# Kernel tuning notes

Hardware: AMD Instinct MI355X
Metric: run time of the kernel (lower is better)

The kernel has to match this reference:

```python
import jax, jax.numpy as jnp
import numpy as np

EMBED_DIM = 512
NUM_HEADS = 8
TGT_LEN = 2048
SRC_LEN = 2048
BSZ = 4
W_SCALE = 0.02  # keep pre-softmax logits in a sane range


def setup_inputs() -> dict:
    key = jax.random.key(0)
    ks = jax.random.split(key, 13)
    E = EMBED_DIM
    inp = {
        "query": jax.random.normal(ks[0], (TGT_LEN, BSZ, E), jnp.float32),
        "key": jax.random.normal(ks[1], (SRC_LEN, BSZ, E), jnp.float32),
        "value": jax.random.normal(ks[2], (SRC_LEN, BSZ, E), jnp.float32),
        "attn_mask": jax.random.normal(ks[3], (TGT_LEN, SRC_LEN), jnp.float32),
        # Linear params, torch layout: W is [out, in], y = x @ W.T + b
        "Wq": jax.random.normal(ks[4], (E, E), jnp.float32) * W_SCALE,
        "bq": jax.random.normal(ks[5], (E,), jnp.float32) * W_SCALE,
        "Wk": jax.random.normal(ks[6], (E, E), jnp.float32) * W_SCALE,
        "bk": jax.random.normal(ks[7], (E,), jnp.float32) * W_SCALE,
        "Wv": jax.random.normal(ks[8], (E, E), jnp.float32) * W_SCALE,
        "bv": jax.random.normal(ks[9], (E,), jnp.float32) * W_SCALE,
        "Wo": jax.random.normal(ks[10], (E, E), jnp.float32) * W_SCALE,
        "bo": jax.random.normal(ks[11], (E,), jnp.float32) * W_SCALE,
    }
    return inp


def reference(query, key, value, attn_mask, Wq, bq, Wk, bk, Wv, bv, Wo, bo):
    # QAT quant/dequant stubs are identity in float math; dropout p=0 (eval) is identity.
    T, B, E = query.shape
    S = key.shape[0]
    H = NUM_HEADS
    hd = E // H
    scale = hd ** (-0.5)

    q = query @ Wq.T + bq            # [T, B, E]
    k = key @ Wk.T + bk              # [S, B, E]
    v = value @ Wv.T + bv            # [S, B, E]

    q = q.reshape(T, B, H, hd) * scale
    k = k.reshape(S, B, H, hd)
    v = v.reshape(S, B, H, hd)

    # scores: [B, H, T, S]
    scores = jnp.einsum("tbhd,sbhd->bhts", q, k)
    scores = scores + attn_mask[None, None, :, :]  # mask_add.add (float mask)
    attn = jax.nn.softmax(scores, axis=-1)         # SegmentLUTSoftmax == softmax in float

    out = jnp.einsum("bhts,sbhd->tbhd", attn, v).reshape(T, B, E)
    out = out @ Wo.T + bo                          # out_proj

    # need_weights=True, average_attn_weights=True: mean over heads -> [B, T, S]
    attn_weights = jnp.sum(attn, axis=1) * (1.0 / H)
    return out, attn_weights
```

## Files before the change

### kernel.cpp

```cpp
#include <hip/hip_runtime.h>
#include <hip/hip_bf16.h>

#define T_LEN 2048
#define S_LEN 2048
#define BSZ   4
#define EMB   512
#define NHEAD 8
#define HDIM  64
#define L2E   1.44269504088896f

using bf16x8 = __attribute__((ext_vector_type(8))) short;
using f32x4  = __attribute__((ext_vector_type(4))) float;

static __device__ __forceinline__ unsigned short f2bf(float x) {
    __hip_bfloat16 h = __float2bfloat16(x);
    return *reinterpret_cast<unsigned short*>(&h);
}
static __device__ __forceinline__ float bf2f(unsigned short u) {
    __hip_bfloat16 h;
    *reinterpret_cast<unsigned short*>(&h) = u;
    return __bfloat162float(h);
}
static __device__ __forceinline__ unsigned int pk2(float a, float b) {
    return (unsigned)f2bf(a) | ((unsigned)f2bf(b) << 16);
}

__global__ __launch_bounds__(256) void convert_w4(
    const float* __restrict__ W0, const float* __restrict__ W1,
    const float* __restrict__ W2, const float* __restrict__ W3,
    unsigned short* __restrict__ Hi, unsigned short* __restrict__ Lo, int n4)
{
    const int z = blockIdx.y;
    const float* X = (z == 0) ? W0 : (z == 1) ? W1 : (z == 2) ? W2 : W3;
    unsigned short* H = Hi + (size_t)z * (size_t)EMB * EMB;
    unsigned short* L = Lo + (size_t)z * (size_t)EMB * EMB;
    const int stride = gridDim.x * 256;
    for (int i = blockIdx.x * 256 + threadIdx.x; i < n4; i += stride) {
        float4 v = ((const float4*)X)[i];
        unsigned short h0 = f2bf(v.x), h1 = f2bf(v.y), h2 = f2bf(v.z), h3 = f2bf(v.w);
        uint2 ph, pg;
        ph.x = (unsigned)h0 | ((unsigned)h1 << 16);
        ph.y = (unsigned)h2 | ((unsigned)h3 << 16);
        pg.x = pk2(v.x - bf2f(h0), v.y - bf2f(h1));
        pg.y = pk2(v.z - bf2f(h2), v.w - bf2f(h3));
        ((uint2*)H)[i] = ph;
        ((uint2*)L)[i] = pg;
    }
}

template <int MODE, bool XF32, bool SPLIT>
__global__ __launch_bounds__(256) void proj_mfma(
    const float* __restrict__ Xf,
    const unsigned short* __restrict__ Xhi, const unsigned short* __restrict__ Xlo,
    const unsigned short* __restrict__ Whi, const unsigned short* __restrict__ Wlo,
    const float* __restrict__ bias,
    float* __restrict__ Yf, unsigned short* __restrict__ Yhi, float scale)
{
    const int n0 = blockIdx.x * 64;
    const int m0 = blockIdx.y * 64;

    __shared__ unsigned short whs[64 * 64];
    __shared__ unsigned short wls[SPLIT ? 64 * 64 : 1];
    __shared__ unsigned short xhs[XF32 ? 64 * 64 : 1];
    __shared__ unsigned short xls[(XF32 && SPLIT) ? 64 * 64 : 1];

    const int tid = threadIdx.x;
    const int w   = tid >> 6;
    const int l   = tid & 63;
    const int l4  = l >> 4, l15 = l & 15;
    const int sw  = (l & 7) << 4;
    char* whsb = (char*)whs;
    char* wlsb = (char*)wls;
    char* xhsb = (char*)xhs;
    char* xlsb = (char*)xls;

    const int srow = tid >> 2;
    const int schk = tid & 3;
    const size_t wbase = (size_t)(n0 + srow) * 512 + schk * 16;
    const int stw = (srow * 128 + schk * 32) ^ ((srow & 7) << 4);

    f32x4 acc[4];
    #pragma unroll
    for (int nb = 0; nb < 4; ++nb) { f32x4 z = {0.f, 0.f, 0.f, 0.f}; acc[nb] = z; }

    uint4 wh0 = *(const uint4*)(Whi + wbase);
    uint4 wh1 = *(const uint4*)(Whi + wbase + 8);
    uint4 wl0, wl1;
    if constexpr (SPLIT) {
        wl0 = *(const uint4*)(Wlo + wbase);
        wl1 = *(const uint4*)(Wlo + wbase + 8);
    }

    const size_t xfbase = (size_t)(m0 + srow) * 512 + schk * 16;
    const size_t xbase  = (size_t)(m0 + w * 16 + l15) * 512 + l4 * 8;
    float4 xp0, xp1, xp2, xp3;
    bf16x8 ah0, ah1, al0, al1;
    if constexpr (XF32) {
        xp0 = *(const float4*)(Xf + xfbase);
        xp1 = *(const float4*)(Xf + xfbase + 4);
        xp2 = *(const float4*)(Xf + xfbase + 8);
        xp3 = *(const float4*)(Xf + xfbase + 12);
    } else {
        ah0 = *(const bf16x8*)(Xhi + xbase);
        ah1 = *(const bf16x8*)(Xhi + xbase + 32);
        if constexpr (SPLIT) {
            al0 = *(const bf16x8*)(Xlo + xbase);
            al1 = *(const bf16x8*)(Xlo + xbase + 32);
        }
    }

    for (int c = 0; c < 8; ++c) {
        __syncthreads();
        *(uint4*)(whsb + stw)        = wh0;
        *(uint4*)(whsb + (stw ^ 16)) = wh1;
        if constexpr (SPLIT) {
            *(uint4*)(wlsb + stw)        = wl0;
            *(uint4*)(wlsb + (stw ^ 16)) = wl1;
        }
        if constexpr (XF32) {
            uint4 H0, H1;
            H0.x = pk2(xp0.x, xp0.y); H0.y = pk2(xp0.z, xp0.w);
            H0.z = pk2(xp1.x, xp1.y); H0.w = pk2(xp1.z, xp1.w);
            H1.x = pk2(xp2.x, xp2.y); H1.y = pk2(xp2.z, xp2.w);
            H1.z = pk2(xp3.x, xp3.y); H1.w = pk2(xp3.z, xp3.w);
            *(uint4*)(xhsb + stw)        = H0;
            *(uint4*)(xhsb + (stw ^ 16)) = H1;
            if constexpr (SPLIT) {
                uint4 L0, L1;
                L0.x = pk2(xp0.x - bf2f(f2bf(xp0.x)), xp0.y - bf2f(f2bf(xp0.y)));
                L0.y = pk2(xp0.z - bf2f(f2bf(xp0.z)), xp0.w - bf2f(f2bf(xp0.w)));
                L0.z = pk2(xp1.x - bf2f(f2bf(xp1.x)), xp1.y - bf2f(f2bf(xp1.y)));
                L0.w = pk2(xp1.z - bf2f(f2bf(xp1.z)), xp1.w - bf2f(f2bf(xp1.w)));
                L1.x = pk2(xp2.x - bf2f(f2bf(xp2.x)), xp2.y - bf2f(f2bf(xp2.y)));
                L1.y = pk2(xp2.z - bf2f(f2bf(xp2.z)), xp2.w - bf2f(f2bf(xp2.w)));
                L1.z = pk2(xp3.x - bf2f(f2bf(xp3.x)), xp3.y - bf2f(f2bf(xp3.y)));
                L1.w = pk2(xp3.z - bf2f(f2bf(xp3.z)), xp3.w - bf2f(f2bf(xp3.w)));
                *(uint4*)(xlsb + stw)        = L0;
                *(uint4*)(xlsb + (stw ^ 16)) = L1;
            }
        }
        __syncthreads();

        bf16x8 cah[2], cal[2];
        if constexpr (XF32) {
            #pragma unroll
            for (int kc = 0; kc < 2; ++kc) {
                const int aoff = (((w * 16 + l15) * 128) + kc * 64 + l4 * 16) ^ sw;
                cah[kc] = *(const bf16x8*)(xhsb + aoff);
                if constexpr (SPLIT) cal[kc] = *(const bf16x8*)(xlsb + aoff);
            }
        } else {
            cah[0] = ah0; cah[1] = ah1;
            if constexpr (SPLIT) { cal[0] = al0; cal[1] = al1; }
        }

        if (c < 7) {
            const size_t wb2 = wbase + (size_t)(c + 1) * 64;
            wh0 = *(const uint4*)(Whi + wb2);
            wh1 = *(const uint4*)(Whi + wb2 + 8);
            if constexpr (SPLIT) {
                wl0 = *(const uint4*)(Wlo + wb2);
                wl1 = *(const uint4*)(Wlo + wb2 + 8);
            }
            if constexpr (XF32) {
                const size_t xb2 = xfbase + (size_t)(c + 1) * 64;
                xp0 = *(const float4*)(Xf + xb2);
                xp1 = *(const float4*)(Xf + xb2 + 4);
                xp2 = *(const float4*)(Xf + xb2 + 8);
                xp3 = *(const float4*)(Xf + xb2 + 12);
            } else {
                const size_t xb2 = xbase + (size_t)(c + 1) * 64;
                ah0 = *(const bf16x8*)(Xhi + xb2);
                ah1 = *(const bf16x8*)(Xhi + xb2 + 32);
                if constexpr (SPLIT) {
                    al0 = *(const bf16x8*)(Xlo + xb2);
                    al1 = *(const bf16x8*)(Xlo + xb2 + 32);
                }
            }
        }

        #pragma unroll
        for (int kc = 0; kc < 2; ++kc) {
            #pragma unroll
            for (int nb = 0; nb < 4; ++nb) {
                const int off = (((nb * 16 + l15) * 128) + kc * 64 + l4 * 16) ^ sw;
                bf16x8 bh = *(const bf16x8*)(whsb + off);
                acc[nb] = __builtin_amdgcn_mfma_f32_16x16x32_bf16(cah[kc], bh, acc[nb], 0, 0, 0);
                if constexpr (SPLIT) {
                    bf16x8 bl = *(const bf16x8*)(wlsb + off);
                    acc[nb] = __builtin_amdgcn_mfma_f32_16x16x32_bf16(cah[kc], bl, acc[nb], 0, 0, 0);
                    acc[nb] = __builtin_amdgcn_mfma_f32_16x16x32_bf16(cal[kc], bh, acc[nb], 0, 0, 0);
                }
            }
        }
    }

    #pragma unroll
    for (int nb = 0; nb < 4; ++nb)
        #pragma unroll
        for (int r = 0; r < 4; ++r) {
            const int m = m0 + w * 16 + l4 * 4 + r;
            const int n = n0 + nb * 16 + l15;
            const float y = (acc[nb][r] + bias[n]) * scale;
            const size_t idx = (size_t)m * 512 + n;
            if constexpr (MODE == 0) Yf[idx] = y;
            else                     Yhi[idx] = f2bf(y);
        }
}

__global__ __launch_bounds__(256) void transpose_v(const unsigned short* __restrict__ V,
                                                   unsigned short* __restrict__ Vt)
{
    const int s0 = blockIdx.x * 64;
    const int h  = blockIdx.y, b = blockIdx.z;
    __shared__ unsigned short tile[64][72];
    const int tid = threadIdx.x;
    {
        const int r = tid >> 2, c = (tid & 3) * 16;
        const unsigned short* src = V + ((size_t)(s0 + r) * BSZ + b) * EMB + h * HDIM + c;
        uint4 u0 = *(const uint4*)(src);
        uint4 u1 = *(const uint4*)(src + 8);
        *(uint4*)&tile[r][c]     = u0;
        *(uint4*)&tile[r][c + 8] = u1;
    }
    __syncthreads();
    {
        const int d = tid >> 2, sg = tid & 3;
        unsigned int w_[8];
        #pragma unroll
        for (int j = 0; j < 8; ++j) {
            unsigned int lo = tile[sg * 16 + 2 * j][d];
            unsigned int hi = tile[sg * 16 + 2 * j + 1][d];
            w_[j] = lo | (hi << 16);
        }
        uint4 o0 = {w_[0], w_[1], w_[2], w_[3]};
        uint4 o1 = {w_[4], w_[5], w_[6], w_[7]};
        unsigned short* dst = Vt + ((size_t)(b * NHEAD + h) * HDIM + d) * S_LEN + s0 + sg * 16;
        *(uint4*)dst       = o0;
        *(uint4*)(dst + 8) = o1;
    }
}

__global__ __launch_bounds__(256) void flash_fwd_mfma(
    const unsigned short* __restrict__ Qbf, const unsigned short* __restrict__ Kbf,
    const unsigned short* __restrict__ Vt,  const float* __restrict__ mask,
    unsigned short* __restrict__ Ohi, unsigned short* __restrict__ Olo,
    float* __restrict__ Lout)
{
    const int tt0 = blockIdx.x * 128;
    const int h   = blockIdx.y, b = blockIdx.z;

    __shared__ unsigned short ks[64 * 64];
    __shared__ unsigned short vs[64 * 64];
    __shared__ unsigned short pl[4][2][16 * 64];

    const int tid = threadIdx.x;
    const int w   = tid >> 6;
    const int l   = tid & 63;
    const int l4  = l >> 4, l15 = l & 15;
    const int sw  = (l & 7) << 4;

    char* ksb = (char*)ks;
    char* vsb = (char*)vs;
    char* pb_[2] = {(char*)pl[w][0], (char*)pl[w][1]};

    bf16x8 qf[2][2];
    #pragma unroll
    for (int a = 0; a < 2; ++a) {
        const int t = tt0 + w * 32 + a * 16 + l15;
        const unsigned short* qp = Qbf + ((size_t)t * BSZ + b) * EMB + h * HDIM + l4 * 8;
        qf[a][0] = *(const bf16x8*)(qp);
        qf[a][1] = *(const bf16x8*)(qp + 32);
    }

    f32x4 oacc[2][4];
    #pragma unroll
    for (int a = 0; a < 2; ++a)
        #pragma unroll
        for (int nb = 0; nb < 4; ++nb) { f32x4 z = {0.f, 0.f, 0.f, 0.f}; oacc[a][nb] = z; }
    float lsum[2] = {0.f, 0.f};

    const int srow = tid >> 2;
    const int schk = tid & 3;
    const unsigned short* kcol = Kbf + (size_t)b * EMB + h * HDIM + schk * 16;
    const unsigned short* vrow = Vt + ((size_t)(b * NHEAD + h) * HDIM + srow) * S_LEN + schk * 16;
    const int stw = (srow * 128 + schk * 32) ^ ((srow & 7) << 4);

    const float* mrowp[2];
    #pragma unroll
    for (int a = 0; a < 2; ++a)
        mrowp[a] = mask + (size_t)(tt0 + w * 32 + a * 16 + l15) * S_LEN + l4 * 4;

    const unsigned short* kp0 = kcol + (size_t)srow * BSZ * EMB;
    uint4 ka0 = *(const uint4*)(kp0);
    uint4 ka1 = *(const uint4*)(kp0 + 8);
    uint4 va0 = *(const uint4*)(vrow);
    uint4 va1 = *(const uint4*)(vrow + 8);

    for (int s0 = 0; s0 < S_LEN; s0 += 64) {
        __syncthreads();
        *(uint4*)(ksb + stw)        = ka0;
        *(uint4*)(ksb + (stw ^ 16)) = ka1;
        *(uint4*)(vsb + stw)        = va0;
        *(uint4*)(vsb + (stw ^ 16)) = va1;
        __syncthreads();

        if (s0 + 64 < S_LEN) {
            const unsigned short* kp2 = kcol + (size_t)(s0 + 64 + srow) * BSZ * EMB;
            ka0 = *(const uint4*)(kp2);
            ka1 = *(const uint4*)(kp2 + 8);
            va0 = *(const uint4*)(vrow + s0 + 64);
            va1 = *(const uint4*)(vrow + s0 + 64 + 8);
        }

        f32x4 sacc[2][4];
        #pragma unroll
        for (int a = 0; a < 2; ++a)
            #pragma unroll
            for (int nb = 0; nb < 4; ++nb) { f32x4 z = {0.f, 0.f, 0.f, 0.f}; sacc[a][nb] = z; }
        #pragma unroll
        for (int kc = 0; kc < 2; ++kc) {
            #pragma unroll
            for (int nb = 0; nb < 4; ++nb) {
                const int off = (((nb * 16 + l15) * 128) + kc * 64 + l4 * 16) ^ sw;
                bf16x8 kf = *(const bf16x8*)(ksb + off);
                sacc[0][nb] = __builtin_amdgcn_mfma_f32_16x16x32_bf16(kf, qf[0][kc], sacc[0][nb], 0, 0, 0);
                sacc[1][nb] = __builtin_amdgcn_mfma_f32_16x16x32_bf16(kf, qf[1][kc], sacc[1][nb], 0, 0, 0);
            }
        }

        #pragma unroll
        for (int a = 0; a < 2; ++a) {
            char* pw = pb_[a];
            #pragma unroll
            for (int nb = 0; nb < 4; ++nb) {
                float4 mk = *(const float4*)(mrowp[a] + s0 + nb * 16);
                const float p0 = __builtin_amdgcn_exp2f(fmaf(mk.x, L2E, sacc[a][nb][0]));
                const float p1 = __builtin_amdgcn_exp2f(fmaf(mk.y, L2E, sacc[a][nb][1]));
                const float p2 = __builtin_amdgcn_exp2f(fmaf(mk.z, L2E, sacc[a][nb][2]));
                const float p3 = __builtin_amdgcn_exp2f(fmaf(mk.w, L2E, sacc[a][nb][3]));
                lsum[a] += (p0 + p1) + (p2 + p3);
                uint2 pk;
                pk.x = pk2(p0, p1);
                pk.y = pk2(p2, p3);
                *(uint2*)(pw + ((l15 * 128 + nb * 32 + l4 * 8) ^ sw)) = pk;
            }
        }

        bf16x8 pa[2][2];
        #pragma unroll
        for (int a = 0; a < 2; ++a) {
            pa[a][0] = *(const bf16x8*)(pb_[a] + ((l15 * 128 + l4 * 16) ^ sw));
            pa[a][1] = *(const bf16x8*)(pb_[a] + ((l15 * 128 + 64 + l4 * 16) ^ sw));
        }
        #pragma unroll
        for (int nb = 0; nb < 4; ++nb) {
            const int off0 = (((nb * 16 + l15) * 128) + l4 * 16) ^ sw;
            bf16x8 vf0 = *(const bf16x8*)(vsb + off0);
            bf16x8 vf1 = *(const bf16x8*)(vsb + (off0 ^ 64));
            oacc[0][nb] = __builtin_amdgcn_mfma_f32_16x16x32_bf16(pa[0][0], vf0, oacc[0][nb], 0, 0, 0);
            oacc[0][nb] = __builtin_amdgcn_mfma_f32_16x16x32_bf16(pa[0][1], vf1, oacc[0][nb], 0, 0, 0);
            oacc[1][nb] = __builtin_amdgcn_mfma_f32_16x16x32_bf16(pa[1][0], vf0, oacc[1][nb], 0, 0, 0);
            oacc[1][nb] = __builtin_amdgcn_mfma_f32_16x16x32_bf16(pa[1][1], vf1, oacc[1][nb], 0, 0, 0);
        }
    }

    #pragma unroll
    for (int a = 0; a < 2; ++a) {
        float lfull = lsum[a];
        lfull += __shfl_xor(lfull, 16);
        lfull += __shfl_xor(lfull, 32);
        float linv[4];
        #pragma unroll
        for (int r = 0; r < 4; ++r)
            linv[r] = 1.0f / __shfl(lfull, l4 * 4 + r);

        #pragma unroll
        for (int nb = 0; nb < 4; ++nb)
            #pragma unroll
            for (int r = 0; r < 4; ++r) {
                const int t = tt0 + w * 32 + a * 16 + l4 * 4 + r;
                const size_t idx = ((size_t)t * BSZ + b) * EMB + h * HDIM + nb * 16 + l15;
                const float y = oacc[a][nb][r] * linv[r];
                const unsigned short hi = f2bf(y);
                Ohi[idx] = hi;
                Olo[idx] = f2bf(y - bf2f(hi));
            }
        if (l < 16)
            Lout[((size_t)b * NHEAD + h) * T_LEN + tt0 + w * 32 + a * 16 + l] = lfull;
    }
}

__global__ __launch_bounds__(256) void attn_weights_mfma(
    const unsigned short* __restrict__ Qhi, const unsigned short* __restrict__ Khi,
    const float* __restrict__ mask, const float* __restrict__ Lin,
    float* __restrict__ Wout)
{
    const int tt0 = blockIdx.x * 128;
    const int ss0 = blockIdx.y * 64;
    const int b   = blockIdx.z;

    __shared__ unsigned short khs[2][64 * 64];
    __shared__ float lls[NHEAD][128];

    const int tid = threadIdx.x;
    const int w   = tid >> 6;
    const int l   = tid & 63;
    const int l4  = l >> 4, l15 = l & 15;
    const int sw  = (l & 7) << 4;

    for (int i = tid; i < NHEAD * 128; i += 256) {
        const int hh = i >> 7, t2 = i & 127;
        lls[hh][t2] = (1.0f / NHEAD) / Lin[(size_t)(b * NHEAD + hh) * T_LEN + tt0 + t2];
    }

    float4 msk[2][4];
    #pragma unroll
    for (int a = 0; a < 2; ++a) {
        const float* mrowp = mask + (size_t)(tt0 + w * 32 + a * 16 + l15) * S_LEN + ss0 + l4 * 4;
        #pragma unroll
        for (int nb = 0; nb < 4; ++nb) msk[a][nb] = *(const float4*)(mrowp + nb * 16);
    }
    #pragma unroll
    for (int a = 0; a < 2; ++a)
        #pragma unroll
        for (int nb = 0; nb < 4; ++nb) {
            msk[a][nb].x *= L2E; msk[a][nb].y *= L2E;
            msk[a][nb].z *= L2E; msk[a][nb].w *= L2E;
        }

    float4 wacc[2][4] = {};

    const int srow = tid >> 2;
    const int schk = tid & 3;
    const size_t kbase = ((size_t)(ss0 + srow) * BSZ + b) * EMB + schk * 16;
    const int stw = (srow * 128 + schk * 32) ^ ((srow & 7) << 4);
    size_t qbase[2];
    #pragma unroll
    for (int a = 0; a < 2; ++a)
        qbase[a] = ((size_t)(tt0 + w * 32 + a * 16 + l15) * BSZ + b) * EMB + l4 * 8;

    {
        uint4 a0 = *(const uint4*)(Khi + kbase);
        uint4 a1 = *(const uint4*)(Khi + kbase + 8);
        char* k0 = (char*)khs[0];
        *(uint4*)(k0 + stw)        = a0;
        *(uint4*)(k0 + (stw ^ 16)) = a1;
    }
    __syncthreads();

    uint4 kh0, kh1;

    for (int h = 0; h < NHEAD; ++h) {
        const int cur = h & 1;
        char* khsb = (char*)khs[cur];
        const bool haveNext = (h + 1 < NHEAD);

        if (haveNext) {
            kh0 = *(const uint4*)(Khi + kbase + (h + 1) * HDIM);
            kh1 = *(const uint4*)(Khi + kbase + (h + 1) * HDIM + 8);
        }

        bf16x8 qh[2][2];
        #pragma unroll
        for (int a = 0; a < 2; ++a) {
            qh[a][0] = *(const bf16x8*)(Qhi + qbase[a] + h * HDIM);
            qh[a][1] = *(const bf16x8*)(Qhi + qbase[a] + h * HDIM + 32);
        }

        f32x4 sacc[2][4];
        #pragma unroll
        for (int a = 0; a < 2; ++a)
            #pragma unroll
            for (int nb = 0; nb < 4; ++nb) { f32x4 z = {0.f, 0.f, 0.f, 0.f}; sacc[a][nb] = z; }
        #pragma unroll
        for (int kc = 0; kc < 2; ++kc) {
            #pragma unroll
            for (int nb = 0; nb < 4; ++nb) {
                const int off = (((nb * 16 + l15) * 128) + kc * 64 + l4 * 16) ^ sw;
                bf16x8 kf = *(const bf16x8*)(khsb + off);
                sacc[0][nb] = __builtin_amdgcn_mfma_f32_16x16x32_bf16(kf, qh[0][kc], sacc[0][nb], 0, 0, 0);
                sacc[1][nb] = __builtin_amdgcn_mfma_f32_16x16x32_bf16(kf, qh[1][kc], sacc[1][nb], 0, 0, 0);
            }
        }

        #pragma unroll
        for (int a = 0; a < 2; ++a) {
            const float lh = lls[h][w * 32 + a * 16 + l15];
            #pragma unroll
            for (int nb = 0; nb < 4; ++nb) {
                wacc[a][nb].x += __builtin_amdgcn_exp2f(sacc[a][nb][0] + msk[a][nb].x) * lh;
                wacc[a][nb].y += __builtin_amdgcn_exp2f(sacc[a][nb][1] + msk[a][nb].y) * lh;
                wacc[a][nb].z += __builtin_amdgcn_exp2f(sacc[a][nb][2] + msk[a][nb].z) * lh;
                wacc[a][nb].w += __builtin_amdgcn_exp2f(sacc[a][nb][3] + msk[a][nb].w) * lh;
            }
        }

        if (haveNext) {
            char* kn = (char*)khs[cur ^ 1];
            *(uint4*)(kn + stw)        = kh0;
            *(uint4*)(kn + (stw ^ 16)) = kh1;
        }
        __syncthreads();
    }

    #pragma unroll
    for (int a = 0; a < 2; ++a) {
        float* orow = Wout + ((size_t)b * T_LEN + tt0 + w * 32 + a * 16 + l15) * S_LEN + ss0 + l4 * 4;
        #pragma unroll
        for (int nb = 0; nb < 4; ++nb)
            *(float4*)(orow + nb * 16) = wacc[a][nb];
    }
}

extern "C" void kernel_launch(void* const* d_in, const int* in_sizes, int n_in,
                              void* d_out, int out_size, void* d_ws, size_t ws_size,
                              hipStream_t stream)
{
    const float* query = (const float*)d_in[0];
    const float* key   = (const float*)d_in[1];
    const float* value = (const float*)d_in[2];
    const float* mask  = (const float*)d_in[3];
    const float* Wq    = (const float*)d_in[4];
    const float* bq    = (const float*)d_in[5];
    const float* Wk    = (const float*)d_in[6];
    const float* bk    = (const float*)d_in[7];
    const float* Wv    = (const float*)d_in[8];
    const float* bv    = (const float*)d_in[9];
    const float* Wo    = (const float*)d_in[10];
    const float* bo    = (const float*)d_in[11];

    float* out = (float*)d_out;

    const size_t NQKV = (size_t)T_LEN * BSZ * EMB;
    const size_t NW   = (size_t)EMB * EMB;

    unsigned short* qhi = (unsigned short*)d_ws;
    unsigned short* khi = qhi + NQKV;
    unsigned short* vhi = khi + NQKV;
    unsigned short* whb = vhi + NQKV;
    unsigned short* wlb = whb + 4 * NW;
    float* lb = (float*)(wlb + 4 * NW);

    unsigned short* wqh = whb + 0 * NW;
    unsigned short* wkh = whb + 1 * NW;
    unsigned short* wvh = whb + 2 * NW;
    unsigned short* woh = whb + 3 * NW, *wol = wlb + 3 * NW;

    unsigned short* vt  = (unsigned short*)(out + NQKV);
    unsigned short* cxh = (unsigned short*)(out + NQKV + 3000000);
    unsigned short* cxl = (unsigned short*)(out + NQKV + 6000000);

    const dim3 gproj(8, 128);

    convert_w4<<<dim3(64, 4), 256, 0, stream>>>(Wq, Wk, Wv, Wo, whb, wlb, (int)(NW / 4));

    proj_mfma<2, true, false><<<gproj, 256, 0, stream>>>(query, nullptr, nullptr, wqh, nullptr,
                                                         bq, nullptr, qhi, 0.125f * L2E);
    proj_mfma<2, true, false><<<gproj, 256, 0, stream>>>(key, nullptr, nullptr, wkh, nullptr,
                                                         bk, nullptr, khi, 1.0f);
    proj_mfma<2, true, false><<<gproj, 256, 0, stream>>>(value, nullptr, nullptr, wvh, nullptr,
                                                         bv, nullptr, vhi, 1.0f);

    transpose_v<<<dim3(S_LEN / 64, NHEAD, BSZ), 256, 0, stream>>>(vhi, vt);

    flash_fwd_mfma<<<dim3(T_LEN / 128, NHEAD, BSZ), 256, 0, stream>>>(
        qhi, khi, vt, mask, cxh, cxl, lb);

    proj_mfma<0, false, true><<<gproj, 256, 0, stream>>>(nullptr, cxh, cxl, woh, wol, bo,
                                                         out, nullptr, 1.0f);

    attn_weights_mfma<<<dim3(T_LEN / 128, S_LEN / 64, BSZ), 256, 0, stream>>>(
        qhi, khi, mask, lb, out + NQKV);
}
```

Measured before the change: 249.7 us.

## Split flash attention KV range across two wave groups with LDS reduction

```diff
diff --git a/kernel.cpp b/kernel.cpp
--- a/kernel.cpp
+++ b/kernel.cpp
@@ -241,7 +241,7 @@
     }
 }
 
-__global__ __launch_bounds__(256) void flash_fwd_mfma(
+__global__ __launch_bounds__(512) void flash_fwd_mfma(
     const unsigned short* __restrict__ Qbf, const unsigned short* __restrict__ Kbf,
     const unsigned short* __restrict__ Vt,  const float* __restrict__ mask,
     unsigned short* __restrict__ Ohi, unsigned short* __restrict__ Olo,
@@ -250,24 +250,26 @@
     const int tt0 = blockIdx.x * 128;
     const int h   = blockIdx.y, b = blockIdx.z;
 
-    __shared__ unsigned short ks[64 * 64];
-    __shared__ unsigned short vs[64 * 64];
-    __shared__ unsigned short pl[4][2][16 * 64];
+    __shared__ unsigned short ks[2][64 * 64];
+    __shared__ unsigned short vs[2][64 * 64];
+    __shared__ unsigned short pl[8][2][16 * 64];
 
     const int tid = threadIdx.x;
     const int w   = tid >> 6;
+    const int sg  = w >> 2;
+    const int wq  = w & 3;
     const int l   = tid & 63;
     const int l4  = l >> 4, l15 = l & 15;
     const int sw  = (l & 7) << 4;
 
-    char* ksb = (char*)ks;
-    char* vsb = (char*)vs;
+    char* ksb = (char*)ks[sg];
+    char* vsb = (char*)vs[sg];
     char* pb_[2] = {(char*)pl[w][0], (char*)pl[w][1]};
 
     bf16x8 qf[2][2];
     #pragma unroll
     for (int a = 0; a < 2; ++a) {
-        const int t = tt0 + w * 32 + a * 16 + l15;
+        const int t = tt0 + wq * 32 + a * 16 + l15;
         const unsigned short* qp = Qbf + ((size_t)t * BSZ + b) * EMB + h * HDIM + l4 * 8;
         qf[a][0] = *(const bf16x8*)(qp);
         qf[a][1] = *(const bf16x8*)(qp + 32);
@@ -280,8 +282,10 @@
         for (int nb = 0; nb < 4; ++nb) { f32x4 z = {0.f, 0.f, 0.f, 0.f}; oacc[a][nb] = z; }
     float lsum[2] = {0.f, 0.f};
 
-    const int srow = tid >> 2;
-    const int schk = tid & 3;
+    const int t256 = tid & 255;
+    const int srow = t256 >> 2;
+    const int schk = t256 & 3;
+    const int sbase = sg * (S_LEN / 2);
     const unsigned short* kcol = Kbf + (size_t)b * EMB + h * HDIM + schk * 16;
     const unsigned short* vrow = Vt + ((size_t)(b * NHEAD + h) * HDIM + srow) * S_LEN + schk * 16;
     const int stw = (srow * 128 + schk * 32) ^ ((srow & 7) << 4);
@@ -289,15 +293,15 @@
     const float* mrowp[2];
     #pragma unroll
     for (int a = 0; a < 2; ++a)
-        mrowp[a] = mask + (size_t)(tt0 + w * 32 + a * 16 + l15) * S_LEN + l4 * 4;
-
-    const unsigned short* kp0 = kcol + (size_t)srow * BSZ * EMB;
+        mrowp[a] = mask + (size_t)(tt0 + wq * 32 + a * 16 + l15) * S_LEN + l4 * 4;
+
+    const unsigned short* kp0 = kcol + (size_t)(sbase + srow) * BSZ * EMB;
     uint4 ka0 = *(const uint4*)(kp0);
     uint4 ka1 = *(const uint4*)(kp0 + 8);
-    uint4 va0 = *(const uint4*)(vrow);
-    uint4 va1 = *(const uint4*)(vrow + 8);
-
-    for (int s0 = 0; s0 < S_LEN; s0 += 64) {
+    uint4 va0 = *(const uint4*)(vrow + sbase);
+    uint4 va1 = *(const uint4*)(vrow + sbase + 8);
+
+    for (int s0 = sbase; s0 < sbase + S_LEN / 2; s0 += 64) {
         __syncthreads();
         *(uint4*)(ksb + stw)        = ka0;
         *(uint4*)(ksb + (stw ^ 16)) = ka1;
@@ -305,7 +309,7 @@
         *(uint4*)(vsb + (stw ^ 16)) = va1;
         __syncthreads();
 
-        if (s0 + 64 < S_LEN) {
+        if (s0 + 64 < sbase + S_LEN / 2) {
             const unsigned short* kp2 = kcol + (size_t)(s0 + 64 + srow) * BSZ * EMB;
             ka0 = *(const uint4*)(kp2);
             ka1 = *(const uint4*)(kp2 + 8);
@@ -365,29 +369,56 @@
         }
     }
 
-    #pragma unroll
-    for (int a = 0; a < 2; ++a) {
-        float lfull = lsum[a];
-        lfull += __shfl_xor(lfull, 16);
-        lfull += __shfl_xor(lfull, 32);
-        float linv[4];
-        #pragma unroll
-        for (int r = 0; r < 4; ++r)
-            linv[r] = 1.0f / __shfl(lfull, l4 * 4 + r);
-
-        #pragma unroll
-        for (int nb = 0; nb < 4; ++nb)
-            #pragma unroll
-            for (int r = 0; r < 4; ++r) {
-                const int t = tt0 + w * 32 + a * 16 + l4 * 4 + r;
-                const size_t idx = ((size_t)t * BSZ + b) * EMB + h * HDIM + nb * 16 + l15;
-                const float y = oacc[a][nb][r] * linv[r];
-                const unsigned short hi = f2bf(y);
-                Ohi[idx] = hi;
-                Olo[idx] = f2bf(y - bf2f(hi));
-            }
-        if (l < 16)
-            Lout[((size_t)b * NHEAD + h) * T_LEN + tt0 + w * 32 + a * 16 + l] = lfull;
+    __syncthreads();
+    float* osc = (float*)pl;
+    float* lsc = (float*)ks;
+    if (sg == 1) {
+        #pragma unroll
+        for (int a = 0; a < 2; ++a) {
+            #pragma unroll
+            for (int nb = 0; nb < 4; ++nb)
+                #pragma unroll
+                for (int r = 0; r < 4; ++r)
+                    osc[wq * 2048 + (a * 16 + nb * 4 + r) * 64 + l] = oacc[a][nb][r];
+            lsc[wq * 128 + a * 64 + l] = lsum[a];
+        }
+    }
+    __syncthreads();
+    if (sg == 0) {
+        #pragma unroll
+        for (int a = 0; a < 2; ++a) {
+            #pragma unroll
+            for (int nb = 0; nb < 4; ++nb)
+                #pragma unroll
+                for (int r = 0; r < 4; ++r)
+                    oacc[a][nb][r] += osc[wq * 2048 + (a * 16 + nb * 4 + r) * 64 + l];
+            lsum[a] += lsc[wq * 128 + a * 64 + l];
+        }
+
+        #pragma unroll
+        for (int a = 0; a < 2; ++a) {
+            float lfull = lsum[a];
+            lfull += __shfl_xor(lfull, 16);
+            lfull += __shfl_xor(lfull, 32);
+            float linv[4];
+            #pragma unroll
+            for (int r = 0; r < 4; ++r)
+                linv[r] = 1.0f / __shfl(lfull, l4 * 4 + r);
+
+            #pragma unroll
+            for (int nb = 0; nb < 4; ++nb)
+                #pragma unroll
+                for (int r = 0; r < 4; ++r) {
+                    const int t = tt0 + wq * 32 + a * 16 + l4 * 4 + r;
+                    const size_t idx = ((size_t)t * BSZ + b) * EMB + h * HDIM + nb * 16 + l15;
+                    const float y = oacc[a][nb][r] * linv[r];
+                    const unsigned short hi = f2bf(y);
+                    Ohi[idx] = hi;
+                    Olo[idx] = f2bf(y - bf2f(hi));
+                }
+            if (l < 16)
+                Lout[((size_t)b * NHEAD + h) * T_LEN + tt0 + wq * 32 + a * 16 + l] = lfull;
+        }
     }
 }
 
@@ -564,7 +595,7 @@
 
     transpose_v<<<dim3(S_LEN / 64, NHEAD, BSZ), 256, 0, stream>>>(vhi, vt);
 
-    flash_fwd_mfma<<<dim3(T_LEN / 128, NHEAD, BSZ), 256, 0, stream>>>(
+    flash_fwd_mfma<<<dim3(T_LEN / 128, NHEAD, BSZ), 512, 0, stream>>>(
         qhi, khi, vt, mask, cxh, cxl, lb);
 
     proj_mfma<0, false, true><<<gproj, 256, 0, stream>>>(nullptr, cxh, cxl, woh, wol, bo,
```

Result: slower. 296.5 us (+18.7%).
